# Kernel tuning notes

Measured on AMD Instinct MI355X. Metric: run time of the kernel, lower is better.

Reference implementation:

```python
import jax, jax.numpy as jnp
import numpy as np

B, N, K, NB = 8, 4096, 16, 8
MAX_RADIUS = 10.0
OUT_MUL = 64  # irreps_out = '64x1o' -> output dim 64*3 = 192


def setup_inputs() -> dict:
    key = jax.random.key(0)
    k1, k2 = jax.random.split(key)
    coords = jax.random.normal(k1, (B, N, 3), dtype=jnp.float32)
    tp_weight = jax.random.normal(k2, (1, NB, OUT_MUL), dtype=jnp.float32)
    return {"coords": coords, "tp_weight": tp_weight}


def _knn_indices(coords, k):
    # coords: [B, N, 3] -> nbr idx [B, N, k] (no self loops), per-batch kNN
    n = coords.shape[1]
    d2 = jnp.sum((coords[:, :, None, :] - coords[:, None, :, :]) ** 2, axis=-1)  # [B,N,N]
    d2 = jnp.where(jnp.eye(n, dtype=bool)[None], jnp.inf, d2)
    _, idx = jax.lax.top_k(-d2, k)  # k nearest
    return idx


def reference(coords, tp_weight):
    nbr = _knn_indices(coords, K)                                # [B,N,K] int32
    nbr_coords = jax.vmap(lambda c, i: c[i])(coords, nbr)        # [B,N,K,3]
    r = nbr_coords - coords[:, :, None, :]                       # sender - receiver
    dist = jnp.linalg.norm(r, axis=-1, keepdims=True)            # [B,N,K,1]
    rhat = r / (dist + 1e-8)                                     # 1x1o input
    cutoff = jnp.clip(dist / MAX_RADIUS, 0.0, 1.0)
    # gaussian soft one-hot over [0,1] with NB centers
    centers = jnp.linspace(0.0, 1.0, NB, dtype=coords.dtype)
    sigma = 1.0 / NB
    g = jnp.exp(-((cutoff - centers) ** 2) / (2.0 * sigma * sigma))  # [B,N,K,NB]
    s = jnp.sum(g, axis=-1, keepdims=True)
    rb = g / jnp.where(s > 0, s, jnp.ones_like(s))               # 8x0e input
    # FullyConnectedTensorProduct 1x1o x NBx0e -> OUT_MULx1o (shared weights)
    # path normalization: 1/sqrt(mul_in1 * mul_in2) = 1/sqrt(NB)
    alpha = 1.0 / np.sqrt(1 * NB)
    W = tp_weight[0]                                             # [NB, OUT_MUL]
    edge_feat = alpha * jnp.einsum('vw,bnkv,bnkm->bnkwm', W, rb, rhat)  # [B,N,K,64,3]
    # exactly k incoming edges per receiver -> scatter_mean == mean over K
    agg = jnp.mean(edge_feat, axis=2).reshape(B, N, OUT_MUL * 3)  # [B,N,192]
    return agg
```

## Files before the change

kernel.cpp:

```cpp
#include <hip/hip_runtime.h>

typedef unsigned int u32;
typedef unsigned long long u64;
typedef float v2f __attribute__((ext_vector_type(2)));

#define NBATCH 8
#define NPTS   4096
#define NQTOT  (NBATCH * NPTS)
#define KNN    16
#define NBASIS 8
#define OUTM   64
#define NSPLIT 8
#define WIN    (NPTS / NSPLIT)
#define QPB    64
#define TKNN   (QPB * NSPLIT)
#define GRP    8
#define BUFCAP 64
#define ROWSTR 81
#define TOFF   64

#define SENT 0x7f800000ffffffffull

__device__ __forceinline__ void ce(u64& x, u64& y) {
  u64 a = x, b = y;
  bool sw = b < a;
  x = sw ? b : a;
  y = sw ? a : b;
}

template <int N>
__device__ __forceinline__ void oems_sort(u64* a) {
#pragma unroll
  for (int p = 1; p < N; p <<= 1) {
#pragma unroll
    for (int k = p; k >= 1; k >>= 1) {
#pragma unroll
      for (int j = k & (p - 1); j + k < N; j += 2 * k) {
#pragma unroll
        for (int i = 0; i < k; ++i) {
          int lo = i + j, hi = i + j + k;
          if (hi < N && (lo / (2 * p)) == (hi / (2 * p)))
            ce(a[lo], a[hi]);
        }
      }
    }
  }
}

__device__ __forceinline__ void merge16(u64 t[16], const u64 a[16]) {
  u64 m[16];
#pragma unroll
  for (int i = 0; i < 16; ++i) {
    u64 x = t[i], y = a[15 - i];
    m[i] = (x < y) ? x : y;
  }
#pragma unroll
  for (int k = 8; k >= 1; k >>= 1) {
#pragma unroll
    for (int i = 0; i < 16; ++i) {
      if ((i & k) == 0) ce(m[i], m[i | k]);
    }
  }
#pragma unroll
  for (int i = 0; i < 16; ++i) t[i] = m[i];
}

__device__ __forceinline__ v2f d2pair(v2f cx, v2f cy, v2f cz, v2f qx, v2f qy,
                                      v2f qz) {
#pragma clang fp contract(off)
  v2f dx = cx - qx;
  v2f dy = cy - qy;
  v2f dz = cz - qz;
  v2f d2 = (dx * dx + dy * dy) + dz * dz;
  return d2;
}

__global__ __launch_bounds__(TKNN) void se3_kernel(
    const float* __restrict__ Xp, const float* __restrict__ Yp,
    const float* __restrict__ Zp, const float4* __restrict__ cpad,
    const float* __restrict__ Wmat, float* __restrict__ out) {
  __shared__ u64 sBuf[QPB * ROWSTR];
  __shared__ u32 sCnt[QPB];
  __shared__ float sThr[QPB];
  __shared__ float sM[QPB * 25];

  const int b = blockIdx.x;
  const int qg = blockIdx.y;
  const int tid = threadIdx.x;
  const int ql = tid & 63;
  const int sp = tid >> 6;
  const int qi = qg * QPB + ql;
  const int base = b * NPTS;

  if (tid < QPB) sCnt[tid] = 0;

  const float qx = Xp[base + qi];
  const float qy = Yp[base + qi];
  const float qz = Zp[base + qi];
  const v2f qxx = {qx, qx}, qyy = {qy, qy}, qzz = {qz, qz};

  const int wbase = __builtin_amdgcn_readfirstlane(sp * WIN);
  const v2f* xs2 = (const v2f*)(Xp + base + wbase);
  const v2f* ys2 = (const v2f*)(Yp + base + wbase);
  const v2f* zs2 = (const v2f*)(Zp + base + wbase);
  const int sj = qi - wbase;

  {
    u64 s16[16];
    float cd[16];
#pragma unroll
    for (int p = 0; p < 8; ++p) {
      v2f d2 = d2pair(xs2[p], ys2[p], zs2[p], qxx, qyy, qzz);
      cd[2 * p + 0] = d2.x;
      cd[2 * p + 1] = d2.y;
    }
#pragma unroll
    for (int i = 0; i < 16; ++i) {
      u64 v = ((u64)__float_as_uint(cd[i]) << 32) | (u32)(wbase + i);
      s16[i] = (i == sj) ? SENT : v;
    }
    oems_sort<16>(s16);

    if (sp >= 1 && sp <= 4) {
#pragma unroll
      for (int e = 0; e < 16; ++e)
        sBuf[ql * ROWSTR + (sp - 1) * 16 + e] = s16[e];
    }
    __syncthreads();
    if (sp == 0) {
      u64 t16[16];
#pragma unroll
      for (int e = 0; e < 16; ++e) t16[e] = s16[e];
#pragma unroll
      for (int s = 0; s < 4; ++s) {
        u64 a[16];
#pragma unroll
        for (int e = 0; e < 16; ++e) a[e] = sBuf[ql * ROWSTR + s * 16 + e];
        merge16(t16, a);
      }
#pragma unroll
      for (int e = 0; e < 16; ++e) sBuf[ql * ROWSTR + TOFF + e] = t16[e];
    }
    __syncthreads();
    if (sp >= 5) {
#pragma unroll
      for (int e = 0; e < 16; ++e)
        sBuf[ql * ROWSTR + (sp - 5) * 16 + e] = s16[e];
    }
    __syncthreads();
    if (sp == 0) {
      u64 t16[16];
#pragma unroll
      for (int e = 0; e < 16; ++e) t16[e] = sBuf[ql * ROWSTR + TOFF + e];
#pragma unroll
      for (int s = 0; s < 3; ++s) {
        u64 a[16];
#pragma unroll
        for (int e = 0; e < 16; ++e) a[e] = sBuf[ql * ROWSTR + s * 16 + e];
        merge16(t16, a);
      }
#pragma unroll
      for (int e = 0; e < 16; ++e) sBuf[ql * ROWSTR + TOFF + e] = t16[e];
      sThr[ql] = __uint_as_float((u32)(t16[15] >> 32));
    }
    __syncthreads();
  }
  float thr = sThr[ql];

  const int selfgrp = (sj >= 0 && sj < WIN) ? (sj >> 3) : -1;
  const u32 selfbit = 1u << (sj & 7);

#pragma unroll
  for (int ph = 0; ph < 5; ++ph) {
    const int cstart = 16 << ph;
    const int cend = 32 << ph;
    for (int g = cstart; g < cend; g += GRP) {
      v2f d2p[4];
#pragma unroll
      for (int p = 0; p < 4; ++p)
        d2p[p] = d2pair(xs2[(g >> 1) + p], ys2[(g >> 1) + p],
                        zs2[(g >> 1) + p], qxx, qyy, qzz);
      u32 want = 0;
#pragma unroll
      for (int i = 0; i < GRP; ++i)
        want |= (d2p[i >> 1][i & 1] <= thr) ? (1u << i) : 0u;
      if ((g >> 3) == selfgrp) want &= ~selfbit;
      if (__any(want)) {
#pragma unroll
        for (int i = 0; i < GRP; ++i) {
          if (want & (1u << i)) {
            u32 slot = atomicAdd(&sCnt[ql], 1u);
            if (slot < BUFCAP)
              sBuf[ql * ROWSTR + slot] =
                  ((u64)__float_as_uint(d2p[i >> 1][i & 1]) << 32) |
                  (u32)(wbase + g + i);
          }
        }
      }
    }
    __syncthreads();
    if (sp == ph + 1) {
      int n = (int)sCnt[ql];
      n = n < BUFCAP ? n : BUFCAP;
      if (__any(n > 0)) {
        u64 t16[16];
#pragma unroll
        for (int e = 0; e < 16; ++e) t16[e] = sBuf[ql * ROWSTR + TOFF + e];
        for (int k = 0; __any(k < n); k += 16) {
          u64 a[16];
#pragma unroll
          for (int e = 0; e < 16; ++e)
            a[e] = (k + e < n) ? sBuf[ql * ROWSTR + k + e] : SENT;
          oems_sort<16>(a);
          merge16(t16, a);
        }
#pragma unroll
        for (int e = 0; e < 16; ++e) sBuf[ql * ROWSTR + TOFF + e] = t16[e];
        sThr[ql] = __uint_as_float((u32)(t16[15] >> 32));
      }
      sCnt[ql] = 0;
    }
    __syncthreads();
    thr = sThr[ql];
  }

  if (sp < 4) {
    const int k = sp;
    u64 pv[4];
#pragma unroll
    for (int e = 0; e < 4; ++e)
      pv[e] = sBuf[ql * ROWSTR + TOFF + k * 4 + e];
    float4 nc[4];
    float dd[4];
#pragma unroll
    for (int e = 0; e < 4; ++e) {
      nc[e] = cpad[base + (int)(u32)pv[e]];
      dd[e] = __uint_as_float((u32)(pv[e] >> 32));
    }
    float M[24];
#pragma unroll
    for (int j = 0; j < 24; ++j) M[j] = 0.f;
#pragma unroll
    for (int e = 0; e < 4; ++e) {
      float rx = nc[e].x - qx;
      float ry = nc[e].y - qy;
      float rz = nc[e].z - qz;
      float dist = sqrtf(dd[e]);
      float inv = 1.0f / (dist + 1e-8f);
      rx *= inv; ry *= inv; rz *= inv;
      float cut = fminf(dist * 0.1f, 1.0f);
      float g[NBASIS], s = 0.f;
#pragma unroll
      for (int v = 0; v < NBASIS; ++v) {
        float t = cut - (float)v * (1.0f / 7.0f);
        g[v] = __expf(-32.0f * t * t);
        s += g[v];
      }
      float rs = 1.0f / s;
#pragma unroll
      for (int v = 0; v < NBASIS; ++v) {
        float rb = g[v] * rs;
        M[v * 3 + 0] = fmaf(rb, rx, M[v * 3 + 0]);
        M[v * 3 + 1] = fmaf(rb, ry, M[v * 3 + 1]);
        M[v * 3 + 2] = fmaf(rb, rz, M[v * 3 + 2]);
      }
    }
    float* fp = (float*)(sBuf + ql * ROWSTR);
#pragma unroll
    for (int c = 0; c < 24; ++c) fp[k * 25 + c] = M[c];
  }
  __syncthreads();

  {
    const float* fp = (const float*)(sBuf + ql * ROWSTR);
#pragma unroll
    for (int j0 = 0; j0 < 3; ++j0) {
      int j = sp * 3 + j0;
      float s = fp[0 * 25 + j] + fp[1 * 25 + j] + fp[2 * 25 + j] +
                fp[3 * 25 + j];
      sM[ql * 25 + j] = s;
    }
  }
  __syncthreads();

  float wreg[NBASIS];
#pragma unroll
  for (int v = 0; v < NBASIS; ++v) wreg[v] = Wmat[v * OUTM + ql];
  const float scale = 0.022097086912079608f;
#pragma unroll
  for (int i = 0; i < 8; ++i) {
    int q = sp * 8 + i;
    const float* mq = sM + q * 25;
    float a0 = 0.f, a1 = 0.f, a2 = 0.f;
#pragma unroll
    for (int v = 0; v < NBASIS; ++v) {
      a0 = fmaf(wreg[v], mq[v * 3 + 0], a0);
      a1 = fmaf(wreg[v], mq[v * 3 + 1], a1);
      a2 = fmaf(wreg[v], mq[v * 3 + 2], a2);
    }
    size_t o = (size_t)(base + qg * QPB + q) * (OUTM * 3) + ql * 3;
    out[o + 0] = a0 * scale;
    out[o + 1] = a1 * scale;
    out[o + 2] = a2 * scale;
  }
}

__global__ void prep_kernel(const float* __restrict__ coords,
                            float* __restrict__ Xp, float* __restrict__ Yp,
                            float* __restrict__ Zp, float4* __restrict__ cpad) {
  int i = blockIdx.x * 256 + threadIdx.x;
  if (i < NQTOT) {
    float x = coords[3 * i + 0];
    float y = coords[3 * i + 1];
    float z = coords[3 * i + 2];
    Xp[i] = x; Yp[i] = y; Zp[i] = z;
    cpad[i] = make_float4(x, y, z, 0.f);
  }
}

extern "C" void kernel_launch(void* const* d_in, const int* in_sizes, int n_in,
                              void* d_out, int out_size, void* d_ws, size_t ws_size,
                              hipStream_t stream) {
  const float* coords = (const float*)d_in[0];
  const float* Wmat = (const float*)d_in[1];
  float* out = (float*)d_out;

  char* w = (char*)d_ws;
  float* Xp = (float*)(w);
  float* Yp = (float*)(w + 131072);
  float* Zp = (float*)(w + 262144);
  float4* cpad = (float4*)(w + 393216);

  prep_kernel<<<dim3((NQTOT + 255) / 256), dim3(256), 0, stream>>>(coords, Xp, Yp, Zp, cpad);
  se3_kernel<<<dim3(NBATCH, NPTS / QPB), dim3(TKNN), 0, stream>>>(Xp, Yp, Zp, cpad, Wmat, out);
}
```

Baseline: 179.4 us.

## Prefilter kNN candidates with dot-product test using precomputed half norms

```diff
diff --git a/kernel.cpp b/kernel.cpp
--- a/kernel.cpp
+++ b/kernel.cpp
@@ -2,7 +2,6 @@
 
 typedef unsigned int u32;
 typedef unsigned long long u64;
-typedef float v2f __attribute__((ext_vector_type(2)));
 
 #define NBATCH 8
 #define NPTS   4096
@@ -14,10 +13,11 @@
 #define WIN    (NPTS / NSPLIT)
 #define QPB    64
 #define TKNN   (QPB * NSPLIT)
-#define GRP    8
+#define GRP    16
 #define BUFCAP 64
 #define ROWSTR 81
 #define TOFF   64
+#define MARGIN 1e-4f
 
 #define SENT 0x7f800000ffffffffull
 
@@ -65,20 +65,18 @@
   for (int i = 0; i < 16; ++i) t[i] = m[i];
 }
 
-__device__ __forceinline__ v2f d2pair(v2f cx, v2f cy, v2f cz, v2f qx, v2f qy,
-                                      v2f qz) {
-#pragma clang fp contract(off)
-  v2f dx = cx - qx;
-  v2f dy = cy - qy;
-  v2f dz = cz - qz;
-  v2f d2 = (dx * dx + dy * dy) + dz * dz;
-  return d2;
+__device__ __forceinline__ float d2exact(float qx, float qy, float qz,
+                                         float cx, float cy, float cz) {
+  float dx = __fadd_rn(qx, -cx);
+  float dy = __fadd_rn(qy, -cy);
+  float dz = __fadd_rn(qz, -cz);
+  return __fadd_rn(__fadd_rn(__fmul_rn(dx, dx), __fmul_rn(dy, dy)),
+                   __fmul_rn(dz, dz));
 }
 
 __global__ __launch_bounds__(TKNN) void se3_kernel(
-    const float* __restrict__ Xp, const float* __restrict__ Yp,
-    const float* __restrict__ Zp, const float4* __restrict__ cpad,
-    const float* __restrict__ Wmat, float* __restrict__ out) {
+    const float4* __restrict__ cpad, const float* __restrict__ Wmat,
+    float* __restrict__ out) {
   __shared__ u64 sBuf[QPB * ROWSTR];
   __shared__ u32 sCnt[QPB];
   __shared__ float sThr[QPB];
@@ -94,29 +92,21 @@
 
   if (tid < QPB) sCnt[tid] = 0;
 
-  const float qx = Xp[base + qi];
-  const float qy = Yp[base + qi];
-  const float qz = Zp[base + qi];
-  const v2f qxx = {qx, qx}, qyy = {qy, qy}, qzz = {qz, qz};
+  const float4 qv = cpad[base + qi];
+  const float qx = qv.x, qy = qv.y, qz = qv.z;
+  const float q2 = 2.0f * qv.w;
 
   const int wbase = __builtin_amdgcn_readfirstlane(sp * WIN);
-  const v2f* xs2 = (const v2f*)(Xp + base + wbase);
-  const v2f* ys2 = (const v2f*)(Yp + base + wbase);
-  const v2f* zs2 = (const v2f*)(Zp + base + wbase);
+  const float4* cp4 = cpad + base + wbase;
   const int sj = qi - wbase;
 
   {
     u64 s16[16];
-    float cd[16];
-#pragma unroll
-    for (int p = 0; p < 8; ++p) {
-      v2f d2 = d2pair(xs2[p], ys2[p], zs2[p], qxx, qyy, qzz);
-      cd[2 * p + 0] = d2.x;
-      cd[2 * p + 1] = d2.y;
-    }
 #pragma unroll
     for (int i = 0; i < 16; ++i) {
-      u64 v = ((u64)__float_as_uint(cd[i]) << 32) | (u32)(wbase + i);
+      float4 c = cp4[i];
+      float d2 = d2exact(qx, qy, qz, c.x, c.y, c.z);
+      u64 v = ((u64)__float_as_uint(d2) << 32) | (u32)(wbase + i);
       s16[i] = (i == sj) ? SENT : v;
     }
     oems_sort<16>(s16);
@@ -166,34 +156,37 @@
     __syncthreads();
   }
   float thr = sThr[ql];
-
-  const int selfgrp = (sj >= 0 && sj < WIN) ? (sj >> 3) : -1;
-  const u32 selfbit = 1u << (sj & 7);
+  float Kq = 0.5f * (q2 - thr - MARGIN);
 
 #pragma unroll
   for (int ph = 0; ph < 5; ++ph) {
     const int cstart = 16 << ph;
     const int cend = 32 << ph;
     for (int g = cstart; g < cend; g += GRP) {
-      v2f d2p[4];
-#pragma unroll
-      for (int p = 0; p < 4; ++p)
-        d2p[p] = d2pair(xs2[(g >> 1) + p], ys2[(g >> 1) + p],
-                        zs2[(g >> 1) + p], qxx, qyy, qzz);
-      u32 want = 0;
-#pragma unroll
-      for (int i = 0; i < GRP; ++i)
-        want |= (d2p[i >> 1][i & 1] <= thr) ? (1u << i) : 0u;
-      if ((g >> 3) == selfgrp) want &= ~selfbit;
-      if (__any(want)) {
+      float sv[GRP];
+      float4 cc[GRP];
+      u64 anyG = 0;
+#pragma unroll
+      for (int i = 0; i < GRP; ++i) {
+        float4 c = cp4[g + i];
+        cc[i] = c;
+        float s = __builtin_fmaf(qx, c.x,
+                  __builtin_fmaf(qy, c.y, qz * c.z));
+        sv[i] = s;
+        anyG |= __ballot(s >= Kq + c.w);
+      }
+      if (anyG) {
 #pragma unroll
         for (int i = 0; i < GRP; ++i) {
-          if (want & (1u << i)) {
-            u32 slot = atomicAdd(&sCnt[ql], 1u);
-            if (slot < BUFCAP)
-              sBuf[ql * ROWSTR + slot] =
-                  ((u64)__float_as_uint(d2p[i >> 1][i & 1]) << 32) |
-                  (u32)(wbase + g + i);
+          if (__any(sv[i] >= Kq + cc[i].w)) {
+            float d2 = d2exact(qx, qy, qz, cc[i].x, cc[i].y, cc[i].z);
+            int j = wbase + g + i;
+            if (d2 <= thr && j != qi) {
+              u32 slot = atomicAdd(&sCnt[ql], 1u);
+              if (slot < BUFCAP)
+                sBuf[ql * ROWSTR + slot] =
+                    ((u64)__float_as_uint(d2) << 32) | (u32)j;
+            }
           }
         }
       }
@@ -222,6 +215,7 @@
     }
     __syncthreads();
     thr = sThr[ql];
+    Kq = 0.5f * (q2 - thr - MARGIN);
   }
 
   if (sp < 4) {
@@ -306,15 +300,14 @@
 }
 
 __global__ void prep_kernel(const float* __restrict__ coords,
-                            float* __restrict__ Xp, float* __restrict__ Yp,
-                            float* __restrict__ Zp, float4* __restrict__ cpad) {
+                            float4* __restrict__ cpad) {
   int i = blockIdx.x * 256 + threadIdx.x;
   if (i < NQTOT) {
     float x = coords[3 * i + 0];
     float y = coords[3 * i + 1];
     float z = coords[3 * i + 2];
-    Xp[i] = x; Yp[i] = y; Zp[i] = z;
-    cpad[i] = make_float4(x, y, z, 0.f);
+    float hc = 0.5f * (x * x + y * y + z * z);
+    cpad[i] = make_float4(x, y, z, hc);
   }
 }
 
@@ -325,12 +318,8 @@
   const float* Wmat = (const float*)d_in[1];
   float* out = (float*)d_out;
 
-  char* w = (char*)d_ws;
-  float* Xp = (float*)(w);
-  float* Yp = (float*)(w + 131072);
-  float* Zp = (float*)(w + 262144);
-  float4* cpad = (float4*)(w + 393216);
-
-  prep_kernel<<<dim3((NQTOT + 255) / 256), dim3(256), 0, stream>>>(coords, Xp, Yp, Zp, cpad);
-  se3_kernel<<<dim3(NBATCH, NPTS / QPB), dim3(TKNN), 0, stream>>>(Xp, Yp, Zp, cpad, Wmat, out);
-}
+  float4* cpad = (float4*)d_ws;
+
+  prep_kernel<<<dim3((NQTOT + 255) / 256), dim3(256), 0, stream>>>(coords, cpad);
+  se3_kernel<<<dim3(NBATCH, NPTS / QPB), dim3(TKNN), 0, stream>>>(cpad, Wmat, out);
+}
```

After: 190.1 us. 6.0% more time.
